# Kernel tuning notes

Measured on AMD Instinct MI355X. Metric: run time of the kernel, lower is better.

## Reference

```python
import jax, jax.numpy as jnp
import numpy as np
import math

# Module hyperparameters (from init_kwargs)
T_TOTAL = 1.0
NUM_STEPS = 8          # == len(F), number of time-indexed sub-networks (experts)
D = 1024               # feature dim (shape = [D])
DH = 4096              # hidden dim of each expert MLP
B = 4096               # batch size
H_STEP = T_TOTAL / NUM_STEPS
EIGMIN, EIGINIT, EIGMAX = -1.0, 0.0, 1.0   # spectral_limits=None
INV_SIG_099 = math.log(0.99 / (1 - 0.99))  # shifta/shiftb/scales init (learn flags False)


def setup_inputs() -> dict:
    key = jax.random.key(0)
    ks = jax.random.split(key, 8)
    t = jax.random.uniform(ks[0], (B,), dtype=jnp.float32) * T_TOTAL
    y = jax.random.normal(ks[1], (B, D), dtype=jnp.float32)
    # Per-expert 2-layer MLP params, stacked over the expert axis E
    s1 = 1.0 / math.sqrt(D)
    s2 = 1.0 / math.sqrt(DH)
    W1 = jax.random.normal(ks[2], (NUM_STEPS, D, DH), dtype=jnp.float32) * s1
    b1 = jnp.zeros((NUM_STEPS, DH), dtype=jnp.float32)
    W2 = jax.random.normal(ks[3], (NUM_STEPS, DH, D), dtype=jnp.float32) * s2
    b2 = jnp.zeros((NUM_STEPS, D), dtype=jnp.float32)
    scales = jnp.full((1, D), INV_SIG_099, dtype=jnp.float32)
    shifta = jnp.float32(INV_SIG_099)
    shiftb = jnp.float32(INV_SIG_099)
    return {"t": t, "y": y, "W1": W1, "b1": b1, "W2": W2, "b2": b2,
            "scales": scales, "shifta": shifta, "shiftb": shiftb}


def reference(t, y, W1, b1, W2, b2, scales, shifta, shiftb):
    E = W1.shape[0]
    # t2ind: per-sample expert index, clamped to the last expert
    ind = jnp.minimum((t / H_STEP).astype(jnp.int32), E - 1)          # [B]
    # Run every expert on every sample (dense dispatch), then gather per-sample result.
    hid = jnp.tanh(jnp.einsum('bd,edh->ebh', y, W1) + b1[:, None, :])  # [E,B,DH]
    fe = jnp.einsum('ebh,ehd->ebd', hid, W2) + b2[:, None, :]          # [E,B,D]
    f = jnp.take_along_axis(fe, ind[None, :, None].astype(jnp.int32), axis=0)[0]  # [B,D]
    f = jax.nn.sigmoid(scales) * f
    a = EIGINIT + jax.nn.sigmoid(shifta) * (EIGMIN - EIGINIT)
    b = EIGINIT + jax.nn.sigmoid(shiftb) * (EIGMAX - EIGINIT)
    return 0.5 * ((b - a) * f + (a + b) * y)
```

## Files before the change

kernel.cpp:

```cpp
#include <hip/hip_runtime.h>
#include <hip/hip_bf16.h>
#include <math.h>

#define NEXP 8
#define DIM_D 1024
#define DIM_H 4096
#define NB 4096

typedef __attribute__((ext_vector_type(8))) short short8;
typedef __attribute__((ext_vector_type(4))) float floatx4;

__device__ __forceinline__ unsigned short f2bf(float x) {
  __hip_bfloat16 h = __float2bfloat16(x);
  unsigned short u;
  __builtin_memcpy(&u, &h, 2);
  return u;
}
__device__ __forceinline__ unsigned int pack2bf(float a, float b) {
  return (unsigned int)f2bf(a) | ((unsigned int)f2bf(b) << 16);
}

__device__ __forceinline__ void async_copy16(const void* g, void* l) {
  __builtin_amdgcn_global_load_lds(
      (const __attribute__((address_space(1))) unsigned int*)g,
      (__attribute__((address_space(3))) unsigned int*)l, 16, 0, 0);
}

__global__ void setup_kernel(const float* __restrict__ t,
                             int* __restrict__ offs, int* __restrict__ perm) {
  __shared__ int cnt[NEXP];
  __shared__ int cur[NEXP];
  const int tid = threadIdx.x;
  if (tid < NEXP) cnt[tid] = 0;
  __syncthreads();
  for (int i = tid; i < NB; i += 256) {
    int e = (int)(t[i] * 8.0f);
    e = e < 0 ? 0 : (e > NEXP - 1 ? NEXP - 1 : e);
    atomicAdd(&cnt[e], 1);
  }
  __syncthreads();
  if (tid == 0) {
    int s = 0;
    for (int e = 0; e < NEXP; ++e) { offs[e] = s; cur[e] = s; s += cnt[e]; }
    offs[NEXP] = s;
  }
  __syncthreads();
  for (int i = tid; i < NB; i += 256) {
    int e = (int)(t[i] * 8.0f);
    e = e < 0 ? 0 : (e > NEXP - 1 ? NEXP - 1 : e);
    int slot = atomicAdd(&cur[e], 1);
    perm[slot] = i;
  }
}

__global__ __launch_bounds__(256)
void cvt_kernel(const float* __restrict__ in, __hip_bfloat16* __restrict__ out) {
  const long long i = ((long long)blockIdx.x * 256 + threadIdx.x) * 8;
  const float4 a = *(const float4*)(in + i);
  const float4 b = *(const float4*)(in + i + 4);
  unsigned int r[4];
  r[0] = pack2bf(a.x, a.y);
  r[1] = pack2bf(a.z, a.w);
  r[2] = pack2bf(b.x, b.y);
  r[3] = pack2bf(b.z, b.w);
  *(uint4*)(out + i) = *(const uint4*)r;
}

__global__ __launch_bounds__(256)
void transpose_cvt_kernel(const float* __restrict__ in,
                          __hip_bfloat16* __restrict__ out, int R, int C) {
  __shared__ __align__(16) unsigned int tile[64 * 36];
  const long long base = (long long)blockIdx.z * R * C;
  const int c0 = blockIdx.x * 64;
  const int r0 = blockIdx.y * 64;
  const int t = threadIdx.x;
  {
    const int ir = t >> 2, q = t & 3;
    const float* src = in + base + (long long)(r0 + ir) * C + c0 + q * 16;
    const float4 v0 = *(const float4*)(src);
    const float4 v1 = *(const float4*)(src + 4);
    const float4 v2 = *(const float4*)(src + 8);
    const float4 v3 = *(const float4*)(src + 12);
    unsigned int* dp = &tile[ir * 36 + q * 8];
    dp[0] = pack2bf(v0.x, v0.y);
    dp[1] = pack2bf(v0.z, v0.w);
    dp[2] = pack2bf(v1.x, v1.y);
    dp[3] = pack2bf(v1.z, v1.w);
    dp[4] = pack2bf(v2.x, v2.y);
    dp[5] = pack2bf(v2.z, v2.w);
    dp[6] = pack2bf(v3.x, v3.y);
    dp[7] = pack2bf(v3.z, v3.w);
  }
  __syncthreads();
  {
    const int oc = t >> 2, rq = t & 3;
    __align__(16) unsigned int res[8];
#pragma unroll
    for (int m2 = 0; m2 < 8; ++m2) {
      const int d = rq * 16 + m2 * 2;
      const unsigned int a = tile[d * 36 + (oc >> 1)];
      const unsigned int b = tile[(d + 1) * 36 + (oc >> 1)];
      res[m2] = (oc & 1) ? ((a >> 16) | (b & 0xffff0000u))
                         : ((a & 0xffffu) | (b << 16));
    }
    __hip_bfloat16* dstp = out + base + (long long)(c0 + oc) * R + r0 + rq * 16;
    *(uint4*)dstp = *(const uint4*)&res[0];
    *(uint4*)(dstp + 8) = *(const uint4*)&res[4];
  }
}

template <int MODE>
__global__ __launch_bounds__(256)
void gemm_kernel(const __hip_bfloat16* __restrict__ A,
                 const __hip_bfloat16* __restrict__ BT,
                 const float* __restrict__ bias,
                 const int* __restrict__ offs, const int* __restrict__ perm,
                 void* __restrict__ dstv,
                 const float* __restrict__ yin,
                 const float* __restrict__ scales,
                 const float* __restrict__ shifta,
                 const float* __restrict__ shiftb,
                 int K, int N) {
  const int e  = blockIdx.y >> 5;
  const int mt = blockIdx.y & 31;
  const int off = offs[e];
  const int cnt = offs[e + 1] - off;
  const int m0 = mt * 128;
  if (m0 >= cnt) return;
  const int rows = min(128, cnt - m0);
  const int n0 = blockIdx.x * 128;

  __shared__ __align__(16) __hip_bfloat16 As[128 * 32];
  __shared__ __align__(16) __hip_bfloat16 Bs[128 * 32];
  __shared__ int rowmap[128];

  const int tid = threadIdx.x;
  if (tid < 128) {
    int r = tid < rows ? tid : rows - 1;
    rowmap[tid] = (MODE == 0) ? perm[off + m0 + r] : (off + m0 + r);
  }
  __syncthreads();

  const int w = tid >> 6, l = tid & 63;
  const __hip_bfloat16* aptr[2];
  const __hip_bfloat16* bptr[2];
  {
    const long long bb = (long long)e * N * K + (long long)n0 * K;
#pragma unroll
    for (int r = 0; r < 2; ++r) {
      const int c = w * 2 + r;
      const int row = c * 16 + (l >> 2);
      const int col = (l & 3) * 8;
      aptr[r] = A + (long long)rowmap[row] * K + col;
      bptr[r] = BT + bb + (long long)row * K + col;
    }
  }

  floatx4 acc[4][4];
#pragma unroll
  for (int i = 0; i < 4; ++i)
#pragma unroll
    for (int j = 0; j < 4; ++j) acc[i][j] = (floatx4){0.f, 0.f, 0.f, 0.f};

  const int wm = w >> 1, wn = w & 1;
  const int fr = l & 15;
  const int fk = (l >> 4) * 8;
  const __hip_bfloat16* Afrag = &As[(wm * 64 + fr) * 32 + fk];
  const __hip_bfloat16* Bfrag = &Bs[(wn * 64 + fr) * 32 + fk];

  for (int kt = 0; kt < K; kt += 32) {
#pragma unroll
    for (int r = 0; r < 2; ++r) {
      const int c = w * 2 + r;
      async_copy16(aptr[r], &As[c * 512]);
      async_copy16(bptr[r], &Bs[c * 512]);
      aptr[r] += 32;
      bptr[r] += 32;
    }
    __syncthreads();
    short8 af[4], bf[4];
#pragma unroll
    for (int mi = 0; mi < 4; ++mi) af[mi] = *(const short8*)(Afrag + mi * 16 * 32);
#pragma unroll
    for (int ni = 0; ni < 4; ++ni) bf[ni] = *(const short8*)(Bfrag + ni * 16 * 32);
#pragma unroll
    for (int mi = 0; mi < 4; ++mi)
#pragma unroll
      for (int ni = 0; ni < 4; ++ni)
        acc[mi][ni] = __builtin_amdgcn_mfma_f32_16x16x32_bf16(af[mi], bf[ni],
                                                              acc[mi][ni], 0, 0, 0);
    __syncthreads();
  }

  float av = 0.f, bv = 0.f;
  if (MODE == 1) {
    const float sa = 1.f / (1.f + expf(-shifta[0]));
    const float sb = 1.f / (1.f + expf(-shiftb[0]));
    av = 0.0f + sa * (-1.0f - 0.0f);
    bv = 0.0f + sb * (1.0f - 0.0f);
  }

#pragma unroll
  for (int mi = 0; mi < 4; ++mi) {
#pragma unroll
    for (int r = 0; r < 4; ++r) {
      const int rl = wm * 64 + mi * 16 + (l >> 4) * 4 + r;
      if (rl >= rows) continue;
      const int i = off + m0 + rl;
      const int orig = (MODE == 1) ? perm[i] : 0;
#pragma unroll
      for (int ni = 0; ni < 4; ++ni) {
        const int cg = n0 + wn * 64 + ni * 16 + fr;
        const float x = acc[mi][ni][r] + bias[e * N + cg];
        if (MODE == 0) {
          ((__hip_bfloat16*)dstv)[(long long)i * N + cg] = __float2bfloat16(tanhf(x));
        } else {
          const float sc = 1.f / (1.f + expf(-scales[cg]));
          const float yv = yin[(long long)orig * N + cg];
          const float res = 0.5f * ((bv - av) * sc * x + (av + bv) * yv);
          ((float*)dstv)[(long long)orig * N + cg] = res;
        }
      }
    }
  }
}

extern "C" void kernel_launch(void* const* d_in, const int* in_sizes, int n_in,
                              void* d_out, int out_size, void* d_ws, size_t ws_size,
                              hipStream_t stream) {
  const float* t      = (const float*)d_in[0];
  const float* y      = (const float*)d_in[1];
  const float* W1     = (const float*)d_in[2];
  const float* b1     = (const float*)d_in[3];
  const float* W2     = (const float*)d_in[4];
  const float* b2     = (const float*)d_in[5];
  const float* scales = (const float*)d_in[6];
  const float* shifta = (const float*)d_in[7];
  const float* shiftb = (const float*)d_in[8];

  char* ws = (char*)d_ws;
  __hip_bfloat16* WT  = (__hip_bfloat16*)ws;
  __hip_bfloat16* hid = (__hip_bfloat16*)(ws + (size_t)64 * 1024 * 1024);
  __hip_bfloat16* ybf = (__hip_bfloat16*)(ws + (size_t)96 * 1024 * 1024);
  int* offs = (int*)(ws + (size_t)104 * 1024 * 1024);
  int* perm = offs + 16;

  setup_kernel<<<1, 256, 0, stream>>>(t, offs, perm);

  cvt_kernel<<<(NB * DIM_D) / (256 * 8), 256, 0, stream>>>(y, ybf);

  transpose_cvt_kernel<<<dim3(DIM_H / 64, DIM_D / 64, NEXP), 256, 0, stream>>>(
      W1, WT, DIM_D, DIM_H);
  gemm_kernel<0><<<dim3(DIM_H / 128, NEXP * 32), 256, 0, stream>>>(
      ybf, WT, b1, offs, perm, hid, nullptr, nullptr, nullptr, nullptr,
      DIM_D, DIM_H);
  transpose_cvt_kernel<<<dim3(DIM_D / 64, DIM_H / 64, NEXP), 256, 0, stream>>>(
      W2, WT, DIM_H, DIM_D);
  gemm_kernel<1><<<dim3(DIM_D / 128, NEXP * 32), 256, 0, stream>>>(
      hid, WT, b2, offs, perm, d_out, y, scales, shifta, shiftb,
      DIM_H, DIM_D);
}
```

Before: 552.4 us.

## Double-buffer GEMM LDS tiles with BK=64 and rework transpose staging

The grouped GEMM now uses a 64 KB LDS buffer holding two stages of 128x64 A and B tiles. It prefetches the next K-tile with async global-to-LDS copies while MFMAs run on the current one, and needs only one barrier per iteration. Row gathering is folded into per-thread pointer setup, so the rowmap shared array and its barrier are gone. The transpose kernel now packs row pairs into bf16x2 words before the LDS write, so the read side is a plain strided gather. The larger LDS footprint limits occupancy per CU, which the launch bounds hint of 2 blocks reflects.

```diff
diff --git a/kernel.cpp b/kernel.cpp
--- a/kernel.cpp
+++ b/kernel.cpp
@@ -69,40 +69,34 @@
 __global__ __launch_bounds__(256)
 void transpose_cvt_kernel(const float* __restrict__ in,
                           __hip_bfloat16* __restrict__ out, int R, int C) {
-  __shared__ __align__(16) unsigned int tile[64 * 36];
+  __shared__ unsigned int wbuf[32 * 69];
   const long long base = (long long)blockIdx.z * R * C;
   const int c0 = blockIdx.x * 64;
   const int r0 = blockIdx.y * 64;
   const int t = threadIdx.x;
   {
-    const int ir = t >> 2, q = t & 3;
-    const float* src = in + base + (long long)(r0 + ir) * C + c0 + q * 16;
-    const float4 v0 = *(const float4*)(src);
-    const float4 v1 = *(const float4*)(src + 4);
-    const float4 v2 = *(const float4*)(src + 8);
-    const float4 v3 = *(const float4*)(src + 12);
-    unsigned int* dp = &tile[ir * 36 + q * 8];
-    dp[0] = pack2bf(v0.x, v0.y);
-    dp[1] = pack2bf(v0.z, v0.w);
-    dp[2] = pack2bf(v1.x, v1.y);
-    dp[3] = pack2bf(v1.z, v1.w);
-    dp[4] = pack2bf(v2.x, v2.y);
-    dp[5] = pack2bf(v2.z, v2.w);
-    dp[6] = pack2bf(v3.x, v3.y);
-    dp[7] = pack2bf(v3.z, v3.w);
+    const int p = t >> 3, g = t & 7;
+    const float* s0 = in + base + (long long)(r0 + 2 * p) * C + c0 + g * 8;
+    const float4 a0 = *(const float4*)(s0);
+    const float4 a1 = *(const float4*)(s0 + 4);
+    const float4 b0 = *(const float4*)(s0 + C);
+    const float4 b1v = *(const float4*)(s0 + C + 4);
+    unsigned int* dp = &wbuf[p * 69 + g * 8];
+    dp[0] = pack2bf(a0.x, b0.x);
+    dp[1] = pack2bf(a0.y, b0.y);
+    dp[2] = pack2bf(a0.z, b0.z);
+    dp[3] = pack2bf(a0.w, b0.w);
+    dp[4] = pack2bf(a1.x, b1v.x);
+    dp[5] = pack2bf(a1.y, b1v.y);
+    dp[6] = pack2bf(a1.z, b1v.z);
+    dp[7] = pack2bf(a1.w, b1v.w);
   }
   __syncthreads();
   {
     const int oc = t >> 2, rq = t & 3;
     __align__(16) unsigned int res[8];
 #pragma unroll
-    for (int m2 = 0; m2 < 8; ++m2) {
-      const int d = rq * 16 + m2 * 2;
-      const unsigned int a = tile[d * 36 + (oc >> 1)];
-      const unsigned int b = tile[(d + 1) * 36 + (oc >> 1)];
-      res[m2] = (oc & 1) ? ((a >> 16) | (b & 0xffff0000u))
-                         : ((a & 0xffffu) | (b << 16));
-    }
+    for (int j = 0; j < 8; ++j) res[j] = wbuf[(rq * 8 + j) * 69 + oc];
     __hip_bfloat16* dstp = out + base + (long long)(c0 + oc) * R + r0 + rq * 16;
     *(uint4*)dstp = *(const uint4*)&res[0];
     *(uint4*)(dstp + 8) = *(const uint4*)&res[4];
@@ -110,7 +104,7 @@
 }
 
 template <int MODE>
-__global__ __launch_bounds__(256)
+__global__ __launch_bounds__(256, 2)
 void gemm_kernel(const __hip_bfloat16* __restrict__ A,
                  const __hip_bfloat16* __restrict__ BT,
                  const float* __restrict__ bias,
@@ -130,30 +124,24 @@
   const int rows = min(128, cnt - m0);
   const int n0 = blockIdx.x * 128;
 
-  __shared__ __align__(16) __hip_bfloat16 As[128 * 32];
-  __shared__ __align__(16) __hip_bfloat16 Bs[128 * 32];
-  __shared__ int rowmap[128];
+  __shared__ __align__(16) char lds[65536];
 
   const int tid = threadIdx.x;
-  if (tid < 128) {
-    int r = tid < rows ? tid : rows - 1;
-    rowmap[tid] = (MODE == 0) ? perm[off + m0 + r] : (off + m0 + r);
-  }
-  __syncthreads();
-
   const int w = tid >> 6, l = tid & 63;
-  const __hip_bfloat16* aptr[2];
-  const __hip_bfloat16* bptr[2];
-  {
-    const long long bb = (long long)e * N * K + (long long)n0 * K;
-#pragma unroll
-    for (int r = 0; r < 2; ++r) {
-      const int c = w * 2 + r;
-      const int row = c * 16 + (l >> 2);
-      const int col = (l & 3) * 8;
-      aptr[r] = A + (long long)rowmap[row] * K + col;
-      bptr[r] = BT + bb + (long long)row * K + col;
-    }
+
+  const __hip_bfloat16* aptr[4];
+  const __hip_bfloat16* bptr[4];
+#pragma unroll
+  for (int j = 0; j < 4; ++j) {
+    const int chunk = j * 256 + tid;
+    const int cgrp = chunk >> 9;
+    const int row  = (chunk >> 2) & 127;
+    const int c2   = chunk & 3;
+    const int ra = row < rows ? row : rows - 1;
+    const long long ga = (MODE == 0) ? (long long)perm[off + m0 + ra]
+                                     : (long long)(off + m0 + ra);
+    aptr[j] = A + ga * K + cgrp * 32 + c2 * 8;
+    bptr[j] = BT + ((long long)e * N + n0 + row) * K + cgrp * 32 + c2 * 8;
   }
 
   floatx4 acc[4][4];
@@ -164,32 +152,50 @@
 
   const int wm = w >> 1, wn = w & 1;
   const int fr = l & 15;
-  const int fk = (l >> 4) * 8;
-  const __hip_bfloat16* Afrag = &As[(wm * 64 + fr) * 32 + fk];
-  const __hip_bfloat16* Bfrag = &Bs[(wn * 64 + fr) * 32 + fk];
-
-  for (int kt = 0; kt < K; kt += 32) {
-#pragma unroll
-    for (int r = 0; r < 2; ++r) {
-      const int c = w * 2 + r;
-      async_copy16(aptr[r], &As[c * 512]);
-      async_copy16(bptr[r], &Bs[c * 512]);
-      aptr[r] += 32;
-      bptr[r] += 32;
+  const int fq = l >> 4;
+  const int ldsA = (wm * 64 + fr) * 64 + fq * 16;
+  const int ldsB = 16384 + (wn * 64 + fr) * 64 + fq * 16;
+
+  const int nt = K >> 6;
+
+#pragma unroll
+  for (int j = 0; j < 4; ++j) {
+    async_copy16(aptr[j], lds + j * 4096 + w * 1024);
+    async_copy16(bptr[j], lds + 16384 + j * 4096 + w * 1024);
+    aptr[j] += 64; bptr[j] += 64;
+  }
+  __syncthreads();
+
+  for (int t = 0; t < nt; ++t) {
+    const int cur = (t & 1) << 15;
+    if (t + 1 < nt) {
+      const int nxt = cur ^ 32768;
+#pragma unroll
+      for (int j = 0; j < 4; ++j) {
+        async_copy16(aptr[j], lds + nxt + j * 4096 + w * 1024);
+        async_copy16(bptr[j], lds + nxt + 16384 + j * 4096 + w * 1024);
+        aptr[j] += 64; bptr[j] += 64;
+      }
     }
-    __syncthreads();
-    short8 af[4], bf[4];
-#pragma unroll
-    for (int mi = 0; mi < 4; ++mi) af[mi] = *(const short8*)(Afrag + mi * 16 * 32);
-#pragma unroll
-    for (int ni = 0; ni < 4; ++ni) bf[ni] = *(const short8*)(Bfrag + ni * 16 * 32);
-#pragma unroll
-    for (int mi = 0; mi < 4; ++mi)
+    short8 af[2][4], bf[2][4];
+#pragma unroll
+    for (int ks = 0; ks < 2; ++ks) {
+#pragma unroll
+      for (int mi = 0; mi < 4; ++mi)
+        af[ks][mi] = *(const short8*)(lds + cur + ks * 8192 + mi * 1024 + ldsA);
 #pragma unroll
       for (int ni = 0; ni < 4; ++ni)
-        acc[mi][ni] = __builtin_amdgcn_mfma_f32_16x16x32_bf16(af[mi], bf[ni],
-                                                              acc[mi][ni], 0, 0, 0);
-    __syncthreads();
+        bf[ks][ni] = *(const short8*)(lds + cur + ks * 8192 + ni * 1024 + ldsB);
+    }
+#pragma unroll
+    for (int ks = 0; ks < 2; ++ks)
+#pragma unroll
+      for (int mi = 0; mi < 4; ++mi)
+#pragma unroll
+        for (int ni = 0; ni < 4; ++ni)
+          acc[mi][ni] = __builtin_amdgcn_mfma_f32_16x16x32_bf16(
+              af[ks][mi], bf[ks][ni], acc[mi][ni], 0, 0, 0);
+    if (t + 1 < nt) __syncthreads();
   }
 
   float av = 0.f, bv = 0.f;
@@ -204,7 +210,7 @@
   for (int mi = 0; mi < 4; ++mi) {
 #pragma unroll
     for (int r = 0; r < 4; ++r) {
-      const int rl = wm * 64 + mi * 16 + (l >> 4) * 4 + r;
+      const int rl = wm * 64 + mi * 16 + fq * 4 + r;
       if (rl >= rows) continue;
       const int i = off + m0 + rl;
       const int orig = (MODE == 1) ? perm[i] : 0;
```

Result: faster. 494.1 us (-10.6%).
